# Kernel optimization log

Hardware: AMD Instinct MI355X
Metric: run time of the kernel (lower is better)

The kernel has to match this reference:

```python
import jax, jax.numpy as jnp
import numpy as np
from jax import lax

L, B = 512, 1024          # seq length, batch
E = 64                    # embedding dim == input_size == hidden (code requires input_size==latent)
H = 64                    # hidden/latent size
VOCAB = 32000


def setup_inputs() -> dict:
    key = jax.random.key(0)
    k1, k2, k3, k4, kx = jax.random.split(key, 5)
    s = 1.0 / np.sqrt(E + H)
    return {
        "x": jax.random.randint(kx, (L, B), 0, VOCAB),
        "emb": jax.random.normal(k1, (VOCAB, E), dtype=jnp.float32) * 0.02,
        # Linear(in=E+H, out=H, bias=False); stored as [in, out] so y = xh @ W
        "Wz": jax.random.uniform(k2, (E + H, H), jnp.float32, -s, s),
        "Wr": jax.random.uniform(k3, (E + H, H), jnp.float32, -s, s),
        "Wh": jax.random.uniform(k4, (H + E, H), jnp.float32, -s, s),
    }


def reference(x, emb, Wz, Wr, Wh):
    xe = emb[x]                                  # [L, B, E] embedding lookup
    h0 = jnp.zeros((x.shape[1], Wz.shape[1]), dtype=xe.dtype)

    def step(h, xt):                             # xt: [B, E], h: [B, H]
        xh = jnp.concatenate([xt, h], axis=-1)   # [B, E+H]
        z = jax.nn.sigmoid(xh @ Wz)              # update gate
        r = jax.nn.sigmoid(xh @ Wr)              # reset gate
        hcand = jnp.tanh(jnp.concatenate([r * h, xt], axis=-1) @ Wh)
        hn = (1.0 - z) * h + z * hcand
        return hn, hn

    h_last, outputs = lax.scan(step, h0, xe)     # outputs: [L, B, H]
    return outputs, h_last
```

## Files before the change

kernel.cpp:

```cpp
#include <hip/hip_runtime.h>

#define L_SEQ 512
#define B_SZ  1024
#define HD    64

__device__ __forceinline__ float fast_sigmoid(float x) {
    return __builtin_amdgcn_rcpf(1.0f + __builtin_amdgcn_exp2f(-1.4426950408889634f * x));
}
__device__ __forceinline__ float fast_tanh(float x) {
    return 1.0f - 2.0f * __builtin_amdgcn_rcpf(1.0f + __builtin_amdgcn_exp2f(2.8853900817779268f * x));
}

#define FMA_Q(vq, warr, acc, i0) do {                      \
    acc = fmaf((vq).x, warr[(i0) + 0], acc);               \
    acc = fmaf((vq).y, warr[(i0) + 1], acc);               \
    acc = fmaf((vq).z, warr[(i0) + 2], acc);               \
    acc = fmaf((vq).w, warr[(i0) + 3], acc);               \
} while (0)

__global__ __launch_bounds__(256, 2) void gru_fused_kernel(
    const int* __restrict__ xind, const float* __restrict__ emb,
    const float* __restrict__ Wz, const float* __restrict__ Wr,
    const float* __restrict__ Wh, float* __restrict__ out)
{
    __shared__ float sm_xh[2][128];
    __shared__ float sm_rh[2][64];
    __shared__ float sm_p1[2][2][4][64];
    __shared__ float sm_p2[2][4][64];

    const int j  = threadIdx.x & 63;
    const int cw = threadIdx.x >> 6;
    const int kb = cw * 16;
    const int b0 = blockIdx.x * 2;

    float wzx[16], wzh[16], wrx[16], wrh[16], whr[16], whx[16];
#pragma unroll
    for (int i = 0; i < 16; ++i) {
        wzx[i] = Wz[(kb + i) * 64 + j];
        wzh[i] = Wz[(64 + kb + i) * 64 + j];
        wrx[i] = Wr[(kb + i) * 64 + j];
        wrh[i] = Wr[(64 + kb + i) * 64 + j];
        whr[i] = Wh[(kb + i) * 64 + j];
        whx[i] = Wh[(64 + kb + i) * 64 + j];
    }

    if (cw < 2) {
        sm_xh[cw][64 + j] = 0.0f;
    } else {
        int r = cw - 2;
        int idx = xind[b0 + r];
        sm_xh[r][j] = emb[(size_t)idx * 64 + j];
    }
    __syncthreads();

    float accC[2];
    float z_reg = 0.0f, h_reg = 0.0f;

    for (int t = 0; t < L_SEQ; ++t) {
        float ev = 0.0f;
        if (cw >= 2 && t < L_SEQ - 1) {
            int r = cw - 2;
            int idx = xind[(t + 1) * B_SZ + b0 + r];
            ev = emb[(size_t)idx * 64 + j];
        }

#pragma unroll
        for (int r = 0; r < 2; ++r) {
            const float4* px = (const float4*)(&sm_xh[r][kb]);
            const float4* ph = (const float4*)(&sm_xh[r][64 + kb]);
            float az = 0.0f, ar = 0.0f, ac = 0.0f;
#pragma unroll
            for (int q = 0; q < 4; ++q) {
                const int i0 = 4 * q;
                float4 xq = px[q];
                float4 hq = ph[q];
                FMA_Q(xq, wzx, az, i0);
                FMA_Q(xq, wrx, ar, i0);
                FMA_Q(xq, whx, ac, i0);
                FMA_Q(hq, wzh, az, i0);
                FMA_Q(hq, wrh, ar, i0);
            }
            sm_p1[r][0][cw][j] = az;
            sm_p1[r][1][cw][j] = ar;
            accC[r] = ac;
        }
        __syncthreads();

        {
            int r = cw & 1;
            if (cw < 2) {
                float s = sm_p1[r][0][0][j] + sm_p1[r][0][1][j]
                        + sm_p1[r][0][2][j] + sm_p1[r][0][3][j];
                z_reg = fast_sigmoid(s);
                h_reg = sm_xh[r][64 + j];
            } else {
                float s = sm_p1[r][1][0][j] + sm_p1[r][1][1][j]
                        + sm_p1[r][1][2][j] + sm_p1[r][1][3][j];
                float rr = fast_sigmoid(s);
                sm_rh[r][j] = rr * sm_xh[r][64 + j];
            }
        }
        __syncthreads();

#pragma unroll
        for (int r = 0; r < 2; ++r) {
            const float4* pr = (const float4*)(&sm_rh[r][kb]);
            float a = accC[r];
#pragma unroll
            for (int q = 0; q < 4; ++q) {
                const int i0 = 4 * q;
                float4 rq = pr[q];
                FMA_Q(rq, whr, a, i0);
            }
            sm_p2[r][cw][j] = a;
        }
        __syncthreads();

        if (cw < 2) {
            int r = cw;
            float s = sm_p2[r][0][j] + sm_p2[r][1][j]
                    + sm_p2[r][2][j] + sm_p2[r][3][j];
            float hc = fast_tanh(s);
            float hn = fmaf(z_reg, hc - h_reg, h_reg);
            sm_xh[r][64 + j] = hn;
            out[(size_t)t * (B_SZ * HD) + (size_t)(b0 + r) * HD + j] = hn;
            if (t == L_SEQ - 1)
                out[(size_t)L_SEQ * B_SZ * HD + (size_t)(b0 + r) * HD + j] = hn;
        } else {
            int r = cw - 2;
            if (t < L_SEQ - 1)
                sm_xh[r][j] = ev;
        }
        __syncthreads();
    }
}

extern "C" void kernel_launch(void* const* d_in, const int* in_sizes, int n_in,
                              void* d_out, int out_size, void* d_ws, size_t ws_size,
                              hipStream_t stream) {
    (void)in_sizes; (void)n_in; (void)out_size; (void)d_ws; (void)ws_size;
    const int*   x   = (const int*)  d_in[0];
    const float* emb = (const float*)d_in[1];
    const float* Wz  = (const float*)d_in[2];
    const float* Wr  = (const float*)d_in[3];
    const float* Wh  = (const float*)d_in[4];
    float* out = (float*)d_out;

    gru_fused_kernel<<<dim3(B_SZ / 2), dim3(256), 0, stream>>>(x, emb, Wz, Wr, Wh, out);
}
```

Measured before the change: 765.3 us.

## Assign one wave per gate with full 64-wide weight columns, one row per block

Restructures the GRU kernel so each block handles one batch row with three waves: one computes the z gate, one the r gate, and one the candidate. Each thread keeps full 64-element weight columns in registers, pinned with empty asm. This removes the cross-wave partial-sum reductions and drops a sync per timestep. It also prefetches token indices two steps ahead. In exchange it uses about 128 weight registers per thread and runs each thread through a longer serial dot product, with the third wave idle during the first phase.

```diff
diff --git a/kernel.cpp b/kernel.cpp
--- a/kernel.cpp
+++ b/kernel.cpp
@@ -11,126 +11,96 @@
     return 1.0f - 2.0f * __builtin_amdgcn_rcpf(1.0f + __builtin_amdgcn_exp2f(2.8853900817779268f * x));
 }
 
-#define FMA_Q(vq, warr, acc, i0) do {                      \
-    acc = fmaf((vq).x, warr[(i0) + 0], acc);               \
-    acc = fmaf((vq).y, warr[(i0) + 1], acc);               \
-    acc = fmaf((vq).z, warr[(i0) + 2], acc);               \
-    acc = fmaf((vq).w, warr[(i0) + 3], acc);               \
-} while (0)
+#define PIN(x) asm volatile("" : "+v"(x))
 
-__global__ __launch_bounds__(256, 2) void gru_fused_kernel(
+__device__ __forceinline__ float dot64(const float* sm, const float* w) {
+    const float4* p = (const float4*)sm;
+    float s0 = 0.0f, s1 = 0.0f;
+#pragma unroll
+    for (int q = 0; q < 16; q += 2) {
+        float4 u = p[q];
+        float4 v = p[q + 1];
+        s0 = fmaf(u.x, w[4 * q + 0], s0); s0 = fmaf(u.y, w[4 * q + 1], s0);
+        s0 = fmaf(u.z, w[4 * q + 2], s0); s0 = fmaf(u.w, w[4 * q + 3], s0);
+        s1 = fmaf(v.x, w[4 * q + 4], s1); s1 = fmaf(v.y, w[4 * q + 5], s1);
+        s1 = fmaf(v.z, w[4 * q + 6], s1); s1 = fmaf(v.w, w[4 * q + 7], s1);
+    }
+    return s0 + s1;
+}
+
+__global__ void __launch_bounds__(192)
+__attribute__((amdgpu_waves_per_eu(2, 3)))
+gru_fused_kernel(
     const int* __restrict__ xind, const float* __restrict__ emb,
     const float* __restrict__ Wz, const float* __restrict__ Wr,
     const float* __restrict__ Wh, float* __restrict__ out)
 {
-    __shared__ float sm_xh[2][128];
-    __shared__ float sm_rh[2][64];
-    __shared__ float sm_p1[2][2][4][64];
-    __shared__ float sm_p2[2][4][64];
+    __shared__ float sm_x[64];
+    __shared__ float sm_h[64];
+    __shared__ float sm_rh[64];
+    __shared__ float sm_z[64];
 
     const int j  = threadIdx.x & 63;
-    const int cw = threadIdx.x >> 6;
-    const int kb = cw * 16;
-    const int b0 = blockIdx.x * 2;
+    const int wv = threadIdx.x >> 6;
+    const int b  = blockIdx.x;
 
-    float wzx[16], wzh[16], wrx[16], wrh[16], whr[16], whx[16];
+    const float* W = (wv == 0) ? Wz : (wv == 1) ? Wr : Wh;
+    const int offA = (wv == 2) ? 64 * 64 : 0;
+    const int offB = 64 * 64 - offA;
+
+    float wA[64], wB[64];
 #pragma unroll
-    for (int i = 0; i < 16; ++i) {
-        wzx[i] = Wz[(kb + i) * 64 + j];
-        wzh[i] = Wz[(64 + kb + i) * 64 + j];
-        wrx[i] = Wr[(kb + i) * 64 + j];
-        wrh[i] = Wr[(64 + kb + i) * 64 + j];
-        whr[i] = Wh[(kb + i) * 64 + j];
-        whx[i] = Wh[(64 + kb + i) * 64 + j];
+    for (int k = 0; k < 64; ++k) {
+        wA[k] = W[offA + k * 64 + j];
+        wB[k] = W[offB + k * 64 + j];
     }
+#pragma unroll
+    for (int k = 0; k < 64; ++k) { PIN(wA[k]); PIN(wB[k]); }
 
-    if (cw < 2) {
-        sm_xh[cw][64 + j] = 0.0f;
-    } else {
-        int r = cw - 2;
-        int idx = xind[b0 + r];
-        sm_xh[r][j] = emb[(size_t)idx * 64 + j];
+    int idxn = 0;
+    if (wv == 0) {
+        sm_x[j] = emb[(size_t)xind[b] * HD + j];
+        idxn = xind[B_SZ + b];
+        sm_z[j] = 0.0f;
+    } else if (wv == 1) {
+        sm_h[j] = 0.0f;
+        sm_rh[j] = 0.0f;
     }
     __syncthreads();
 
-    float accC[2];
-    float z_reg = 0.0f, h_reg = 0.0f;
-
+    float* outp = out + (size_t)b * HD + j;
     for (int t = 0; t < L_SEQ; ++t) {
         float ev = 0.0f;
-        if (cw >= 2 && t < L_SEQ - 1) {
-            int r = cw - 2;
-            int idx = xind[(t + 1) * B_SZ + b0 + r];
-            ev = emb[(size_t)idx * 64 + j];
+        int idx2 = idxn;
+        if (wv == 0) {
+            if (t < L_SEQ - 1) ev = emb[(size_t)idxn * HD + j];
+            if (t < L_SEQ - 2) idx2 = xind[(t + 2) * B_SZ + b];
         }
 
-#pragma unroll
-        for (int r = 0; r < 2; ++r) {
-            const float4* px = (const float4*)(&sm_xh[r][kb]);
-            const float4* ph = (const float4*)(&sm_xh[r][64 + kb]);
-            float az = 0.0f, ar = 0.0f, ac = 0.0f;
-#pragma unroll
-            for (int q = 0; q < 4; ++q) {
-                const int i0 = 4 * q;
-                float4 xq = px[q];
-                float4 hq = ph[q];
-                FMA_Q(xq, wzx, az, i0);
-                FMA_Q(xq, wrx, ar, i0);
-                FMA_Q(xq, whx, ac, i0);
-                FMA_Q(hq, wzh, az, i0);
-                FMA_Q(hq, wrh, ar, i0);
-            }
-            sm_p1[r][0][cw][j] = az;
-            sm_p1[r][1][cw][j] = ar;
-            accC[r] = ac;
+        float a0 = dot64(sm_x, wA);
+        if (wv < 2) {
+            float a1 = dot64(sm_h, wB);
+            float g = fast_sigmoid(a0 + a1);
+            if (wv == 0) sm_z[j] = g;
+            else         sm_rh[j] = g * sm_h[j];
         }
         __syncthreads();
 
-        {
-            int r = cw & 1;
-            if (cw < 2) {
-                float s = sm_p1[r][0][0][j] + sm_p1[r][0][1][j]
-                        + sm_p1[r][0][2][j] + sm_p1[r][0][3][j];
-                z_reg = fast_sigmoid(s);
-                h_reg = sm_xh[r][64 + j];
-            } else {
-                float s = sm_p1[r][1][0][j] + sm_p1[r][1][1][j]
-                        + sm_p1[r][1][2][j] + sm_p1[r][1][3][j];
-                float rr = fast_sigmoid(s);
-                sm_rh[r][j] = rr * sm_xh[r][64 + j];
-            }
+        if (wv == 2) {
+            float a2 = dot64(sm_rh, wB);
+            float hc = fast_tanh(a0 + a2);
+            float ho = sm_h[j];
+            float z  = sm_z[j];
+            float hn = fmaf(z, hc - ho, ho);
+            sm_h[j] = hn;
+            outp[0] = hn;
+            if (t == L_SEQ - 1)
+                out[(size_t)L_SEQ * B_SZ * HD + (size_t)b * HD + j] = hn;
+        } else if (wv == 0) {
+            if (t < L_SEQ - 1) sm_x[j] = ev;
+            idxn = idx2;
         }
-        __syncthreads();
-
-#pragma unroll
-        for (int r = 0; r < 2; ++r) {
-            const float4* pr = (const float4*)(&sm_rh[r][kb]);
-            float a = accC[r];
-#pragma unroll
-            for (int q = 0; q < 4; ++q) {
-                const int i0 = 4 * q;
-                float4 rq = pr[q];
-                FMA_Q(rq, whr, a, i0);
-            }
-            sm_p2[r][cw][j] = a;
-        }
-        __syncthreads();
-
-        if (cw < 2) {
-            int r = cw;
-            float s = sm_p2[r][0][j] + sm_p2[r][1][j]
-                    + sm_p2[r][2][j] + sm_p2[r][3][j];
-            float hc = fast_tanh(s);
-            float hn = fmaf(z_reg, hc - h_reg, h_reg);
-            sm_xh[r][64 + j] = hn;
-            out[(size_t)t * (B_SZ * HD) + (size_t)(b0 + r) * HD + j] = hn;
-            if (t == L_SEQ - 1)
-                out[(size_t)L_SEQ * B_SZ * HD + (size_t)(b0 + r) * HD + j] = hn;
-        } else {
-            int r = cw - 2;
-            if (t < L_SEQ - 1)
-                sm_xh[r][j] = ev;
-        }
+        outp += (size_t)B_SZ * HD;
         __syncthreads();
     }
 }
@@ -146,5 +116,5 @@
     const float* Wh  = (const float*)d_in[4];
     float* out = (float*)d_out;
 
-    gru_fused_kernel<<<dim3(B_SZ / 2), dim3(256), 0, stream>>>(x, emb, Wz, Wr, Wh, out);
+    gru_fused_kernel<<<dim3(B_SZ), dim3(192), 0, stream>>>(x, emb, Wz, Wr, Wh, out);
 }
```

Result: slower. 1.078 ms (+40.9%).
